# Kernel tuning notes

Measured on AMD Instinct MI355X. Metric: run time of the kernel, lower is better.

The kernel has to match this reference:

```python
import jax, jax.numpy as jnp
import numpy as np

# Dims: B=256 batch, S=512 src_len, H=512 hidden, E=256 embed, V=16000 vocab, L=1 layer
B, S, H, E, V = 256, 512, 512, 256, 16000


def setup_inputs() -> dict:
    key = jax.random.key(0)
    ks = jax.random.split(key, 12)
    inp = {
        'tgt': jax.random.randint(ks[0], (B, 1), 0, V),
        'hidden': jax.random.normal(ks[1], (1, B, H), jnp.float32),
        'cell': jax.random.normal(ks[2], (1, B, H), jnp.float32),
        'encoder_outputs': jax.random.normal(ks[3], (B, S, H), jnp.float32),
        # parameters
        'emb_table': jax.random.normal(ks[4], (V, E), jnp.float32) * 0.02,
        'attn_W': jax.random.normal(ks[5], (H, 2 * H), jnp.float32) * (1.0 / np.sqrt(2 * H)),
        'attn_b': jnp.zeros((H,), jnp.float32),
        'v': jax.random.uniform(ks[6], (H,), jnp.float32, -1.0 / np.sqrt(H), 1.0 / np.sqrt(H)),
        'W_ih': jax.random.normal(ks[7], (4 * H, E + H), jnp.float32) * (1.0 / np.sqrt(H)),
        'W_hh': jax.random.normal(ks[8], (4 * H, H), jnp.float32) * (1.0 / np.sqrt(H)),
        'b_ih': jnp.zeros((4 * H,), jnp.float32),
        'b_hh': jnp.zeros((4 * H,), jnp.float32),
        'fc_W': jax.random.normal(ks[9], (V, H), jnp.float32) * (1.0 / np.sqrt(H)),
        'fc_b': jnp.zeros((V,), jnp.float32),
    }
    return inp


def reference(tgt, hidden, cell, encoder_outputs, emb_table, attn_W, attn_b, v,
              W_ih, W_hh, b_ih, b_hh, fc_W, fc_b):
    # Embedding (dropout = identity, eval mode)  -> [B, 1, E]
    embedded = emb_table[tgt]
    h = hidden[-1]                                   # [B, H]
    c = cell[-1]                                     # [B, H]

    # Bahdanau additive attention
    Sdim = encoder_outputs.shape[1]
    h_rep = jnp.broadcast_to(h[:, None, :], (h.shape[0], Sdim, h.shape[1]))
    cat = jnp.concatenate([h_rep, encoder_outputs], axis=2)          # [B, S, 2H]
    energy = jnp.tanh(jnp.einsum('bsk,hk->bsh', cat, attn_W) + attn_b)
    scores = jnp.einsum('h,bsh->bs', v, energy)                      # [B, S]
    attn = jax.nn.softmax(scores, axis=1)                            # [B, S]

    # context = bmm(attn[:,None,:], encoder_outputs)  -> [B, H]
    context = jnp.einsum('bs,bsh->bh', attn, encoder_outputs)

    # Single-step LSTM cell (PyTorch gate order i, f, g, o)
    x = jnp.concatenate([embedded[:, 0, :], context], axis=1)        # [B, E+H]
    gates = x @ W_ih.T + b_ih + h @ W_hh.T + b_hh                    # [B, 4H]
    i, f, g, o = jnp.split(gates, 4, axis=1)
    c_new = jax.nn.sigmoid(f) * c + jax.nn.sigmoid(i) * jnp.tanh(g)
    h_new = jax.nn.sigmoid(o) * jnp.tanh(c_new)

    prediction = h_new @ fc_W.T + fc_b                               # [B, V]
    return prediction, h_new[None], c_new[None], attn[:, None, :]
```

## Files before the change

kernel.cpp:

```cpp
#include <hip/hip_runtime.h>
#include <hip/hip_bf16.h>

#define B_ 256
#define S_ 512
#define H_ 512
#define E_ 256
#define V_ 16000

typedef __attribute__((ext_vector_type(4))) float f32x4_t;
typedef __attribute__((ext_vector_type(2))) float f32x2_t;
typedef __attribute__((ext_vector_type(8))) short bf16x8_t;
typedef __attribute__((ext_vector_type(2))) unsigned u32x2_t;
typedef __attribute__((ext_vector_type(4))) unsigned u32x4_t;

#define W2_SCALE 64.0f
#define W2_INV   0.015625f

__device__ __forceinline__ bf16x8_t pack8(f32x4_t a, f32x4_t b) {
    union { unsigned u[4]; bf16x8_t v; } o;
    asm("v_cvt_pk_bf16_f32 %0, %1, %2" : "=v"(o.u[0]) : "v"(a[0]), "v"(a[1]));
    asm("v_cvt_pk_bf16_f32 %0, %1, %2" : "=v"(o.u[1]) : "v"(a[2]), "v"(a[3]));
    asm("v_cvt_pk_bf16_f32 %0, %1, %2" : "=v"(o.u[2]) : "v"(b[0]), "v"(b[1]));
    asm("v_cvt_pk_bf16_f32 %0, %1, %2" : "=v"(o.u[3]) : "v"(b[2]), "v"(b[3]));
    return o.v;
}

__device__ __forceinline__ void cvt8(short* dst, const float* src) {
    f32x4_t a = *(const f32x4_t*)src;
    f32x4_t b = *(const f32x4_t*)(src + 4);
    *(bf16x8_t*)dst = pack8(a, b);
}

__device__ __forceinline__ u32x2_t f32x8_to_fp8x8(f32x4_t a, f32x4_t b, float s) {
    unsigned d0 = 0, d1 = 0;
    d0 = __builtin_amdgcn_cvt_pk_fp8_f32(a[0] * s, a[1] * s, d0, false);
    d0 = __builtin_amdgcn_cvt_pk_fp8_f32(a[2] * s, a[3] * s, d0, true);
    d1 = __builtin_amdgcn_cvt_pk_fp8_f32(b[0] * s, b[1] * s, d1, false);
    d1 = __builtin_amdgcn_cvt_pk_fp8_f32(b[2] * s, b[3] * s, d1, true);
    u32x2_t r; r[0] = d0; r[1] = d1;
    return r;
}

__device__ __forceinline__ float tanh5(float x) {
    float e = __expf(2.f * x);
    return 1.f - 2.f * __builtin_amdgcn_rcpf(e + 1.f);
}

__device__ __forceinline__ int physc(int c, int r) {
    return ((((c & 7) << 3) | (c >> 3)) ^ (r & 7));
}

__global__ void pack_w2(const float* __restrict__ attn_W, unsigned* __restrict__ Bp)
{
    const int u    = blockIdx.x * 256 + threadIdx.x;
    const int lane = u & 63;
    const int p    = (u >> 6) & 1;
    const int wn   = (u >> 7) & 7;
    const int kk   = u >> 10;
    const int col0 = wn * 64 + (2 * p) * 16 + (lane & 15);
    const int k    = kk * 32 + (lane >> 4) * 8;
    const float* s0 = attn_W + (size_t)col0 * (2 * H_) + H_ + k;
    const float* s1 = s0 + (size_t)16 * (2 * H_);
    f32x4_t a0 = *(const f32x4_t*)s0, b0 = *(const f32x4_t*)(s0 + 4);
    f32x4_t a1 = *(const f32x4_t*)s1, b1 = *(const f32x4_t*)(s1 + 4);
    u32x2_t lo = f32x8_to_fp8x8(a0, b0, W2_SCALE);
    u32x2_t hi = f32x8_to_fp8x8(a1, b1, W2_SCALE);
    u32x4_t st; st[0] = lo[0]; st[1] = lo[1]; st[2] = hi[0]; st[3] = hi[1];
    *(u32x4_t*)(Bp + (size_t)u * 4) = st;
}

__global__ void bias1_kernel(const float* __restrict__ hidden,
                             const float* __restrict__ attn_W,
                             const float* __restrict__ attn_b,
                             float* __restrict__ bias1)
{
    const int t  = threadIdx.x;
    const int b0 = blockIdx.x * 2;
    __shared__ float h_s[2][512];
    h_s[0][t] = hidden[(size_t)b0 * H_ + t];
    h_s[1][t] = hidden[(size_t)(b0 + 1) * H_ + t];
    __syncthreads();
    const float* wrow = attn_W + (size_t)t * (2 * H_);
    float a0 = 0.f, a1 = 0.f;
#pragma unroll 4
    for (int k = 0; k < 512; k += 4) {
        f32x4_t wv = *(const f32x4_t*)(wrow + k);
        a0 = fmaf(wv[0], h_s[0][k],     a0);
        a0 = fmaf(wv[1], h_s[0][k + 1], a0);
        a0 = fmaf(wv[2], h_s[0][k + 2], a0);
        a0 = fmaf(wv[3], h_s[0][k + 3], a0);
        a1 = fmaf(wv[0], h_s[1][k],     a1);
        a1 = fmaf(wv[1], h_s[1][k + 1], a1);
        a1 = fmaf(wv[2], h_s[1][k + 2], a1);
        a1 = fmaf(wv[3], h_s[1][k + 3], a1);
    }
    const float bb = attn_b[t];
    bias1[(size_t)b0 * H_ + t]       = a0 + bb;
    bias1[(size_t)(b0 + 1) * H_ + t] = a1 + bb;
}

__global__ void fused_attn(const float* __restrict__ enc,
                           const unsigned* __restrict__ Bp,
                           const float* __restrict__ bias1,
                           const float* __restrict__ vvec,
                           float* __restrict__ e_ws,
                           float* __restrict__ lpart,
                           float* __restrict__ ctxpart)
{
    __shared__ unsigned char buf8[32 * 512];
    __shared__ float bias_s[512];
    __shared__ float v_s[512];
    __shared__ float red[32][9];
    __shared__ float e_loc[32];

    const int t    = threadIdx.x;
    const int lane = t & 63;
    const int w    = t >> 6;
    const int b    = blockIdx.x >> 4;
    const int q    = blockIdx.x & 15;

    bias_s[t] = bias1[(size_t)b * H_ + t];
    v_s[t]    = vvec[t];

    const int srow = t >> 4;
    const int sc   = t & 15;
    const float* gp = enc + ((size_t)b * S_ + q * 32 + srow) * H_ + sc * 32;
#pragma unroll
    for (int i = 0; i < 4; ++i) {
        f32x4_t a = *(const f32x4_t*)(gp + i * 8);
        f32x4_t c = *(const f32x4_t*)(gp + i * 8 + 4);
        *(u32x2_t*)&buf8[srow * 512 + physc(sc * 4 + i, srow) * 8] =
            f32x8_to_fp8x8(a, c, 1.0f);
    }
    __syncthreads();

    const int l15 = lane & 15;
    const int hi  = lane >> 4;
    const int Y   = l15 & 7;
    const unsigned char* abase = buf8 + l15 * 512 + hi * 64;
    const unsigned* bbase = Bp + (size_t)w * 512 + lane * 4;

    f32x4_t acc[2][4];
#pragma unroll
    for (int mf = 0; mf < 2; ++mf)
#pragma unroll
        for (int nf = 0; nf < 4; ++nf)
            acc[mf][nf] = (f32x4_t){0.f, 0.f, 0.f, 0.f};

#pragma unroll
    for (int kk2 = 0; kk2 < 8; ++kk2) {
        const unsigned char* ap = abase + ((kk2 ^ Y) << 3);
        const unsigned* bp = bbase + (size_t)kk2 * 8192;
#pragma unroll
        for (int par = 0; par < 2; ++par) {
            const unsigned char* app = ap + par * 256;
            const unsigned* bpp = bp + par * 4096;
            long a0 = *(const long*)(app);
            long a1 = *(const long*)(app + 8192);
            union { u32x4_t v; long l[2]; } q0, q1;
            q0.v = *(const u32x4_t*)(bpp);
            q1.v = *(const u32x4_t*)(bpp + 256);
            __builtin_amdgcn_s_setprio(1);
            acc[0][0] = __builtin_amdgcn_mfma_f32_16x16x32_fp8_fp8(a0, q0.l[0], acc[0][0], 0, 0, 0);
            acc[1][0] = __builtin_amdgcn_mfma_f32_16x16x32_fp8_fp8(a1, q0.l[0], acc[1][0], 0, 0, 0);
            acc[0][1] = __builtin_amdgcn_mfma_f32_16x16x32_fp8_fp8(a0, q0.l[1], acc[0][1], 0, 0, 0);
            acc[1][1] = __builtin_amdgcn_mfma_f32_16x16x32_fp8_fp8(a1, q0.l[1], acc[1][1], 0, 0, 0);
            acc[0][2] = __builtin_amdgcn_mfma_f32_16x16x32_fp8_fp8(a0, q1.l[0], acc[0][2], 0, 0, 0);
            acc[1][2] = __builtin_amdgcn_mfma_f32_16x16x32_fp8_fp8(a1, q1.l[0], acc[1][2], 0, 0, 0);
            acc[0][3] = __builtin_amdgcn_mfma_f32_16x16x32_fp8_fp8(a0, q1.l[1], acc[0][3], 0, 0, 0);
            acc[1][3] = __builtin_amdgcn_mfma_f32_16x16x32_fp8_fp8(a1, q1.l[1], acc[1][3], 0, 0, 0);
            __builtin_amdgcn_s_setprio(0);
        }
    }

    float part[8];
#pragma unroll
    for (int i = 0; i < 8; ++i) part[i] = 0.f;
#pragma unroll
    for (int nf = 0; nf < 4; ++nf) {
        const int col = w * 64 + nf * 16 + l15;
        const float bbv = bias_s[col];
        const float vl  = v_s[col];
#pragma unroll
        for (int mf = 0; mf < 2; ++mf)
#pragma unroll
            for (int r = 0; r < 4; ++r)
                part[mf * 4 + r] += vl * tanh5(fmaf(acc[mf][nf][r], W2_INV, bbv));
    }
#pragma unroll
    for (int i = 0; i < 8; ++i) {
        float p = part[i];
        p += __shfl_xor(p, 1);
        p += __shfl_xor(p, 2);
        p += __shfl_xor(p, 4);
        p += __shfl_xor(p, 8);
        part[i] = p;
    }
    if (l15 == 0) {
#pragma unroll
        for (int mf = 0; mf < 2; ++mf)
#pragma unroll
            for (int r = 0; r < 4; ++r)
                red[mf * 16 + (hi << 2) + r][w] = part[mf * 4 + r];
    }
    __syncthreads();

    if (t < 32) {
        float s = red[t][0] + red[t][1] + red[t][2] + red[t][3]
                + red[t][4] + red[t][5] + red[t][6] + red[t][7];
        e_loc[t] = __expf(s);
    }
    __syncthreads();

    const int cg = lane >> 3;
    const int cc = (lane & 7) * 8 + w;
    float acc8[8];
#pragma unroll
    for (int j = 0; j < 8; ++j) acc8[j] = 0.f;
#pragma unroll
    for (int i = 0; i < 4; ++i) {
        const int r   = i * 8 + cg;
        const float e = e_loc[r];
        u32x2_t ch = *(const u32x2_t*)&buf8[r * 512 + physc(cc, r) * 8];
        f32x2_t f0 = __builtin_amdgcn_cvt_pk_f32_fp8(ch[0], false);
        f32x2_t f1 = __builtin_amdgcn_cvt_pk_f32_fp8(ch[0], true);
        f32x2_t f2 = __builtin_amdgcn_cvt_pk_f32_fp8(ch[1], false);
        f32x2_t f3 = __builtin_amdgcn_cvt_pk_f32_fp8(ch[1], true);
        acc8[0] = fmaf(e, f0[0], acc8[0]);
        acc8[1] = fmaf(e, f0[1], acc8[1]);
        acc8[2] = fmaf(e, f1[0], acc8[2]);
        acc8[3] = fmaf(e, f1[1], acc8[3]);
        acc8[4] = fmaf(e, f2[0], acc8[4]);
        acc8[5] = fmaf(e, f2[1], acc8[5]);
        acc8[6] = fmaf(e, f3[0], acc8[6]);
        acc8[7] = fmaf(e, f3[1], acc8[7]);
    }
#pragma unroll
    for (int m = 8; m < 64; m <<= 1)
#pragma unroll
        for (int j = 0; j < 8; ++j)
            acc8[j] += __shfl_xor(acc8[j], m);
#pragma unroll
    for (int j = 0; j < 8; ++j)
        if (cg == j)
            ctxpart[(size_t)blockIdx.x * H_ + cc * 8 + j] = acc8[j];

    if (t < 32) {
        float sv = e_loc[t];
        sv += __shfl_xor(sv, 1);
        sv += __shfl_xor(sv, 2);
        sv += __shfl_xor(sv, 4);
        sv += __shfl_xor(sv, 8);
        sv += __shfl_xor(sv, 16);
        if (lane == 0) lpart[blockIdx.x] = sv;
        e_ws[(size_t)b * S_ + q * 32 + t] = e_loc[t];
    }
}

__global__ void combine_kernel(const float* __restrict__ e_ws,
                               const float* __restrict__ lpart,
                               const float* __restrict__ ctxpart,
                               float* __restrict__ out_attn,
                               short* __restrict__ x_cat)
{
    const int b = blockIdx.x, t = threadIdx.x;
    float l = 0.f;
#pragma unroll
    for (int j = 0; j < 16; ++j) l += lpart[16 * b + j];
    const float li = 1.f / l;
    out_attn[(size_t)b * S_ + t] = e_ws[(size_t)b * S_ + t] * li;
    float ctx = 0.f;
#pragma unroll
    for (int j = 0; j < 16; ++j)
        ctx += ctxpart[(size_t)(16 * b + j) * H_ + t];
    union { float f; unsigned u; } v; v.f = ctx * li;
    unsigned r = v.u + 0x7fffu + ((v.u >> 16) & 1u);
    x_cat[(size_t)b * 1280 + 256 + t] = (short)(r >> 16);
}

template<int KIND>
__global__ __launch_bounds__(256, 2)
void gemm_std(const short* __restrict__ Abf,
              const float* __restrict__ B0,
              const float* __restrict__ B1,
              const float* __restrict__ bias0,
              float* __restrict__ out)
{
    constexpr int K = (KIND == 0) ? 1280 : 512;
    constexpr int N = (KIND == 0) ? 2048 : 16000;
    constexpr int KITER = (KIND == 0) ? 20 : 16;

    __shared__ short As[128 * 40];
    __shared__ short Bs[128 * 40];

    const int t    = threadIdx.x;
    const int lane = t & 63;
    const int w    = t >> 6;
    const int wm   = w >> 1;
    const int wn   = w & 1;
    const int row0 = blockIdx.x * 128;
    const int col0 = blockIdx.y * 128;
    const int z    = (KIND == 0) ? blockIdx.z : 0;
    const int ks0  = z * KITER;
    float* outp    = (KIND == 0) ? out + (size_t)z * 256 * 2048 : out;

    f32x4_t acc[4][4];
#pragma unroll
    for (int i = 0; i < 4; ++i)
#pragma unroll
        for (int j = 0; j < 4; ++j)
            acc[i][j] = (f32x4_t){0.f, 0.f, 0.f, 0.f};

    const int arow = t >> 1, ah = (t & 1) * 16;
    const int bcol = t >> 1, bh = (t & 1) * 16;

    for (int ksi = 0; ksi < KITER; ++ksi) {
        const int k0 = (ks0 + ksi) * 32;
        __syncthreads();
        const short* asrc = Abf + (size_t)(row0 + arow) * K + k0 + ah;
        *(bf16x8_t*)&As[arow * 40 + ah]     = *(const bf16x8_t*)asrc;
        *(bf16x8_t*)&As[arow * 40 + ah + 8] = *(const bf16x8_t*)(asrc + 8);
        const float* bsrc;
        if constexpr (KIND == 0) {
            const int cg = col0 + bcol;
            bsrc = (k0 < 768) ? (B0 + (size_t)cg * 768 + k0 + bh)
                              : (B1 + (size_t)cg * 512 + (k0 - 768) + bh);
        } else {
            bsrc = B0 + (size_t)(col0 + bcol) * 512 + k0 + bh;
        }
        cvt8(&Bs[bcol * 40 + bh],     bsrc);
        cvt8(&Bs[bcol * 40 + bh + 8], bsrc + 8);
        __syncthreads();

        bf16x8_t af[4], bfr[4];
        const int ka = (lane >> 4) * 8;
#pragma unroll
        for (int mf = 0; mf < 4; ++mf)
            af[mf] = *(const bf16x8_t*)&As[(wm * 64 + mf * 16 + (lane & 15)) * 40 + ka];
#pragma unroll
        for (int nf = 0; nf < 4; ++nf)
            bfr[nf] = *(const bf16x8_t*)&Bs[(wn * 64 + nf * 16 + (lane & 15)) * 40 + ka];
#pragma unroll
        for (int mf = 0; mf < 4; ++mf)
#pragma unroll
            for (int nf = 0; nf < 4; ++nf)
                acc[mf][nf] = __builtin_amdgcn_mfma_f32_16x16x32_bf16(
                    af[mf], bfr[nf], acc[mf][nf], 0, 0, 0);
    }

#pragma unroll
    for (int mf = 0; mf < 4; ++mf)
#pragma unroll
        for (int nf = 0; nf < 4; ++nf) {
            const int col  = col0 + wn * 64 + nf * 16 + (lane & 15);
            const int rowb = row0 + wm * 64 + mf * 16 + ((lane >> 4) << 2);
#pragma unroll
            for (int r = 0; r < 4; ++r) {
                float v = acc[mf][nf][r];
                if constexpr (KIND == 1) v += bias0[col];
                outp[(size_t)(rowb + r) * N + col] = v;
            }
        }
}

__global__ void prep_kernel(const int* __restrict__ tgt,
                            const float* __restrict__ emb,
                            const float* __restrict__ hidden,
                            short* __restrict__ x_cat)
{
    const int b = blockIdx.x, t = threadIdx.x;
    const int tok = tgt[b];
    union { float f; unsigned u; } v0, v1, v2;
    v0.f = emb[(size_t)tok * E_ + t];
    v1.f = hidden[(size_t)b * H_ + t];
    v2.f = hidden[(size_t)b * H_ + 256 + t];
    unsigned r0 = v0.u + 0x7fffu + ((v0.u >> 16) & 1u);
    unsigned r1 = v1.u + 0x7fffu + ((v1.u >> 16) & 1u);
    unsigned r2 = v2.u + 0x7fffu + ((v2.u >> 16) & 1u);
    x_cat[(size_t)b * 1280 + t]             = (short)(r0 >> 16);
    x_cat[(size_t)b * 1280 + 768 + t]       = (short)(r1 >> 16);
    x_cat[(size_t)b * 1280 + 768 + 256 + t] = (short)(r2 >> 16);
}

__global__ void lstm_kernel(const float* __restrict__ gates0,
                            const float* __restrict__ gates1,
                            const float* __restrict__ b_ih,
                            const float* __restrict__ b_hh,
                            const float* __restrict__ cell,
                            float* __restrict__ out_h,
                            float* __restrict__ out_c,
                            short* __restrict__ h_bf)
{
    const int b = blockIdx.x, t = threadIdx.x;
    const float* g0 = gates0 + (size_t)b * 2048;
    const float* g1 = gates1 + (size_t)b * 2048;
    const float gi = g0[t]        + g1[t]        + b_ih[t]        + b_hh[t];
    const float gf = g0[512 + t]  + g1[512 + t]  + b_ih[512 + t]  + b_hh[512 + t];
    const float gg = g0[1024 + t] + g1[1024 + t] + b_ih[1024 + t] + b_hh[1024 + t];
    const float go = g0[1536 + t] + g1[1536 + t] + b_ih[1536 + t] + b_hh[1536 + t];
    const float c  = cell[(size_t)b * H_ + t];
    const float si = 1.f / (1.f + __expf(-gi));
    const float sf = 1.f / (1.f + __expf(-gf));
    const float so = 1.f / (1.f + __expf(-go));
    const float cn = sf * c + si * tanhf(gg);
    const float hn = so * tanhf(cn);
    out_h[(size_t)b * H_ + t] = hn;
    out_c[(size_t)b * H_ + t] = cn;
    union { float f; unsigned u; } v; v.f = hn;
    unsigned r = v.u + 0x7fffu + ((v.u >> 16) & 1u);
    h_bf[(size_t)b * H_ + t]  = (short)(r >> 16);
}

extern "C" void kernel_launch(void* const* d_in, const int* in_sizes, int n_in,
                              void* d_out, int out_size, void* d_ws, size_t ws_size,
                              hipStream_t stream)
{
    (void)in_sizes; (void)n_in; (void)out_size; (void)ws_size;

    const int*   tgt    = (const int*)d_in[0];
    const float* hidden = (const float*)d_in[1];
    const float* cell   = (const float*)d_in[2];
    const float* enc    = (const float*)d_in[3];
    const float* emb    = (const float*)d_in[4];
    const float* attn_W = (const float*)d_in[5];
    const float* attn_b = (const float*)d_in[6];
    const float* vv     = (const float*)d_in[7];
    const float* W_ih   = (const float*)d_in[8];
    const float* W_hh   = (const float*)d_in[9];
    const float* b_ih   = (const float*)d_in[10];
    const float* b_hh   = (const float*)d_in[11];
    const float* fc_W   = (const float*)d_in[12];
    const float* fc_b   = (const float*)d_in[13];

    float* out_pred = (float*)d_out;
    float* out_h    = out_pred + (size_t)B_ * V_;
    float* out_c    = out_h + (size_t)B_ * H_;
    float* out_attn = out_c + (size_t)B_ * H_;

    char*  ws      = (char*)d_ws;
    float* bias1   = (float*)ws;
    float* gates01 = bias1 + (size_t)B_ * H_;
    float* e_ws    = gates01 + (size_t)2 * B_ * 2048;
    float* lpart   = e_ws + (size_t)B_ * S_;
    float* ctxpart = lpart + 4096;
    short* x_cat   = (short*)(ctxpart + (size_t)4096 * H_);
    short* h_bf    = x_cat + (size_t)B_ * 1280;
    unsigned* b2p  = (unsigned*)(h_bf + (size_t)B_ * H_);

    pack_w2<<<64, 256, 0, stream>>>(attn_W, b2p);
    prep_kernel<<<B_, 256, 0, stream>>>(tgt, emb, hidden, x_cat);
    bias1_kernel<<<128, 512, 0, stream>>>(hidden, attn_W, attn_b, bias1);
    fused_attn<<<16 * B_, 512, 0, stream>>>(enc, b2p, bias1, vv, e_ws, lpart, ctxpart);
    combine_kernel<<<B_, 512, 0, stream>>>(e_ws, lpart, ctxpart, out_attn, x_cat);
    gemm_std<0><<<dim3(2, 16, 2), 256, 0, stream>>>(x_cat, W_ih, W_hh, nullptr, gates01);
    lstm_kernel<<<B_, 512, 0, stream>>>(gates01, gates01 + (size_t)B_ * 2048,
                                        b_ih, b_hh, cell, out_h, out_c, h_bf);
    gemm_std<1><<<dim3(2, 125), 256, 0, stream>>>(h_bf, fc_W, nullptr, fc_b, out_pred);
}
```

Before: 201.5 us.

## Enlarge attention tiles to 64 rows per block with 16 waves

The fused attention kernel now processes 64 source rows per block with 1024 threads instead of 32 rows with 512 threads. Each wave covers 32 hidden columns across four row fragments instead of 64 columns across two. The weight packing layout, the context reduction mapping and the combine kernel are adjusted to match. This halves the number of blocks and the per-block partial context and sum buffers, which cuts workspace traffic in the combine step and improves reuse of the weight fragments. In exchange it uses larger blocks with more LDS, which may reduce the number of blocks resident per CU.

```diff
diff --git a/kernel.cpp b/kernel.cpp
--- a/kernel.cpp
+++ b/kernel.cpp
@@ -54,10 +54,9 @@
 {
     const int u    = blockIdx.x * 256 + threadIdx.x;
     const int lane = u & 63;
-    const int p    = (u >> 6) & 1;
-    const int wn   = (u >> 7) & 7;
+    const int w    = (u >> 6) & 15;
     const int kk   = u >> 10;
-    const int col0 = wn * 64 + (2 * p) * 16 + (lane & 15);
+    const int col0 = w * 32 + (lane & 15);
     const int k    = kk * 32 + (lane >> 4) * 8;
     const float* s0 = attn_W + (size_t)col0 * (2 * H_) + H_ + k;
     const float* s1 = s0 + (size_t)16 * (2 * H_);
@@ -107,24 +106,26 @@
                            float* __restrict__ lpart,
                            float* __restrict__ ctxpart)
 {
-    __shared__ unsigned char buf8[32 * 512];
+    __shared__ unsigned char buf8[64 * 512];
     __shared__ float bias_s[512];
     __shared__ float v_s[512];
-    __shared__ float red[32][9];
-    __shared__ float e_loc[32];
+    __shared__ float red[64][17];
+    __shared__ float e_loc[64];
 
     const int t    = threadIdx.x;
     const int lane = t & 63;
     const int w    = t >> 6;
-    const int b    = blockIdx.x >> 4;
-    const int q    = blockIdx.x & 15;
-
-    bias_s[t] = bias1[(size_t)b * H_ + t];
-    v_s[t]    = vvec[t];
+    const int b    = blockIdx.x >> 3;
+    const int q    = blockIdx.x & 7;
+
+    if (t < 512) {
+        bias_s[t] = bias1[(size_t)b * H_ + t];
+        v_s[t]    = vvec[t];
+    }
 
     const int srow = t >> 4;
     const int sc   = t & 15;
-    const float* gp = enc + ((size_t)b * S_ + q * 32 + srow) * H_ + sc * 32;
+    const float* gp = enc + ((size_t)b * S_ + q * 64 + srow) * H_ + sc * 32;
 #pragma unroll
     for (int i = 0; i < 4; ++i) {
         f32x4_t a = *(const f32x4_t*)(gp + i * 8);
@@ -138,14 +139,14 @@
     const int hi  = lane >> 4;
     const int Y   = l15 & 7;
     const unsigned char* abase = buf8 + l15 * 512 + hi * 64;
-    const unsigned* bbase = Bp + (size_t)w * 512 + lane * 4;
-
-    f32x4_t acc[2][4];
-#pragma unroll
-    for (int mf = 0; mf < 2; ++mf)
-#pragma unroll
-        for (int nf = 0; nf < 4; ++nf)
-            acc[mf][nf] = (f32x4_t){0.f, 0.f, 0.f, 0.f};
+    const unsigned* bbase = Bp + (size_t)w * 256 + lane * 4;
+
+    f32x4_t acc[4][2];
+#pragma unroll
+    for (int mf = 0; mf < 4; ++mf) {
+        acc[mf][0] = (f32x4_t){0.f, 0.f, 0.f, 0.f};
+        acc[mf][1] = (f32x4_t){0.f, 0.f, 0.f, 0.f};
+    }
 
 #pragma unroll
     for (int kk2 = 0; kk2 < 8; ++kk2) {
@@ -154,41 +155,41 @@
 #pragma unroll
         for (int par = 0; par < 2; ++par) {
             const unsigned char* app = ap + par * 256;
-            const unsigned* bpp = bp + par * 4096;
+            union { u32x4_t v; long l[2]; } q0;
+            q0.v = *(const u32x4_t*)(bp + par * 4096);
             long a0 = *(const long*)(app);
             long a1 = *(const long*)(app + 8192);
-            union { u32x4_t v; long l[2]; } q0, q1;
-            q0.v = *(const u32x4_t*)(bpp);
-            q1.v = *(const u32x4_t*)(bpp + 256);
+            long a2 = *(const long*)(app + 16384);
+            long a3 = *(const long*)(app + 24576);
             __builtin_amdgcn_s_setprio(1);
             acc[0][0] = __builtin_amdgcn_mfma_f32_16x16x32_fp8_fp8(a0, q0.l[0], acc[0][0], 0, 0, 0);
             acc[1][0] = __builtin_amdgcn_mfma_f32_16x16x32_fp8_fp8(a1, q0.l[0], acc[1][0], 0, 0, 0);
+            acc[2][0] = __builtin_amdgcn_mfma_f32_16x16x32_fp8_fp8(a2, q0.l[0], acc[2][0], 0, 0, 0);
+            acc[3][0] = __builtin_amdgcn_mfma_f32_16x16x32_fp8_fp8(a3, q0.l[0], acc[3][0], 0, 0, 0);
             acc[0][1] = __builtin_amdgcn_mfma_f32_16x16x32_fp8_fp8(a0, q0.l[1], acc[0][1], 0, 0, 0);
             acc[1][1] = __builtin_amdgcn_mfma_f32_16x16x32_fp8_fp8(a1, q0.l[1], acc[1][1], 0, 0, 0);
-            acc[0][2] = __builtin_amdgcn_mfma_f32_16x16x32_fp8_fp8(a0, q1.l[0], acc[0][2], 0, 0, 0);
-            acc[1][2] = __builtin_amdgcn_mfma_f32_16x16x32_fp8_fp8(a1, q1.l[0], acc[1][2], 0, 0, 0);
-            acc[0][3] = __builtin_amdgcn_mfma_f32_16x16x32_fp8_fp8(a0, q1.l[1], acc[0][3], 0, 0, 0);
-            acc[1][3] = __builtin_amdgcn_mfma_f32_16x16x32_fp8_fp8(a1, q1.l[1], acc[1][3], 0, 0, 0);
+            acc[2][1] = __builtin_amdgcn_mfma_f32_16x16x32_fp8_fp8(a2, q0.l[1], acc[2][1], 0, 0, 0);
+            acc[3][1] = __builtin_amdgcn_mfma_f32_16x16x32_fp8_fp8(a3, q0.l[1], acc[3][1], 0, 0, 0);
             __builtin_amdgcn_s_setprio(0);
         }
     }
 
-    float part[8];
-#pragma unroll
-    for (int i = 0; i < 8; ++i) part[i] = 0.f;
-#pragma unroll
-    for (int nf = 0; nf < 4; ++nf) {
-        const int col = w * 64 + nf * 16 + l15;
+    float part[16];
+#pragma unroll
+    for (int i = 0; i < 16; ++i) part[i] = 0.f;
+#pragma unroll
+    for (int nf = 0; nf < 2; ++nf) {
+        const int col = w * 32 + nf * 16 + l15;
         const float bbv = bias_s[col];
         const float vl  = v_s[col];
 #pragma unroll
-        for (int mf = 0; mf < 2; ++mf)
+        for (int mf = 0; mf < 4; ++mf)
 #pragma unroll
             for (int r = 0; r < 4; ++r)
                 part[mf * 4 + r] += vl * tanh5(fmaf(acc[mf][nf][r], W2_INV, bbv));
     }
 #pragma unroll
-    for (int i = 0; i < 8; ++i) {
+    for (int i = 0; i < 16; ++i) {
         float p = part[i];
         p += __shfl_xor(p, 1);
         p += __shfl_xor(p, 2);
@@ -198,28 +199,29 @@
     }
     if (l15 == 0) {
 #pragma unroll
-        for (int mf = 0; mf < 2; ++mf)
+        for (int mf = 0; mf < 4; ++mf)
 #pragma unroll
             for (int r = 0; r < 4; ++r)
                 red[mf * 16 + (hi << 2) + r][w] = part[mf * 4 + r];
     }
     __syncthreads();
 
-    if (t < 32) {
-        float s = red[t][0] + red[t][1] + red[t][2] + red[t][3]
-                + red[t][4] + red[t][5] + red[t][6] + red[t][7];
+    if (t < 64) {
+        float s = 0.f;
+#pragma unroll
+        for (int g = 0; g < 16; ++g) s += red[t][g];
         e_loc[t] = __expf(s);
     }
     __syncthreads();
 
-    const int cg = lane >> 3;
-    const int cc = (lane & 7) * 8 + w;
+    const int cc = t >> 4;
+    const int rg = t & 15;
     float acc8[8];
 #pragma unroll
     for (int j = 0; j < 8; ++j) acc8[j] = 0.f;
 #pragma unroll
     for (int i = 0; i < 4; ++i) {
-        const int r   = i * 8 + cg;
+        const int r   = i * 16 + rg;
         const float e = e_loc[r];
         u32x2_t ch = *(const u32x2_t*)&buf8[r * 512 + physc(cc, r) * 8];
         f32x2_t f0 = __builtin_amdgcn_cvt_pk_f32_fp8(ch[0], false);
@@ -236,24 +238,25 @@
         acc8[7] = fmaf(e, f3[1], acc8[7]);
     }
 #pragma unroll
-    for (int m = 8; m < 64; m <<= 1)
+    for (int m = 1; m < 16; m <<= 1)
 #pragma unroll
         for (int j = 0; j < 8; ++j)
             acc8[j] += __shfl_xor(acc8[j], m);
 #pragma unroll
     for (int j = 0; j < 8; ++j)
-        if (cg == j)
+        if (rg == j)
             ctxpart[(size_t)blockIdx.x * H_ + cc * 8 + j] = acc8[j];
 
-    if (t < 32) {
+    if (t < 64) {
         float sv = e_loc[t];
         sv += __shfl_xor(sv, 1);
         sv += __shfl_xor(sv, 2);
         sv += __shfl_xor(sv, 4);
         sv += __shfl_xor(sv, 8);
         sv += __shfl_xor(sv, 16);
+        sv += __shfl_xor(sv, 32);
         if (lane == 0) lpart[blockIdx.x] = sv;
-        e_ws[(size_t)b * S_ + q * 32 + t] = e_loc[t];
+        e_ws[(size_t)b * S_ + q * 64 + t] = e_loc[t];
     }
 }
 
@@ -266,13 +269,13 @@
     const int b = blockIdx.x, t = threadIdx.x;
     float l = 0.f;
 #pragma unroll
-    for (int j = 0; j < 16; ++j) l += lpart[16 * b + j];
+    for (int j = 0; j < 8; ++j) l += lpart[8 * b + j];
     const float li = 1.f / l;
     out_attn[(size_t)b * S_ + t] = e_ws[(size_t)b * S_ + t] * li;
     float ctx = 0.f;
 #pragma unroll
-    for (int j = 0; j < 16; ++j)
-        ctx += ctxpart[(size_t)(16 * b + j) * H_ + t];
+    for (int j = 0; j < 8; ++j)
+        ctx += ctxpart[(size_t)(8 * b + j) * H_ + t];
     union { float f; unsigned u; } v; v.f = ctx * li;
     unsigned r = v.u + 0x7fffu + ((v.u >> 16) & 1u);
     x_cat[(size_t)b * 1280 + 256 + t] = (short)(r >> 16);
@@ -442,15 +445,15 @@
     float* gates01 = bias1 + (size_t)B_ * H_;
     float* e_ws    = gates01 + (size_t)2 * B_ * 2048;
     float* lpart   = e_ws + (size_t)B_ * S_;
-    float* ctxpart = lpart + 4096;
-    short* x_cat   = (short*)(ctxpart + (size_t)4096 * H_);
+    float* ctxpart = lpart + 2048;
+    short* x_cat   = (short*)(ctxpart + (size_t)2048 * H_);
     short* h_bf    = x_cat + (size_t)B_ * 1280;
     unsigned* b2p  = (unsigned*)(h_bf + (size_t)B_ * H_);
 
     pack_w2<<<64, 256, 0, stream>>>(attn_W, b2p);
     prep_kernel<<<B_, 256, 0, stream>>>(tgt, emb, hidden, x_cat);
     bias1_kernel<<<128, 512, 0, stream>>>(hidden, attn_W, attn_b, bias1);
-    fused_attn<<<16 * B_, 512, 0, stream>>>(enc, b2p, bias1, vv, e_ws, lpart, ctxpart);
+    fused_attn<<<8 * B_, 1024, 0, stream>>>(enc, b2p, bias1, vv, e_ws, lpart, ctxpart);
     combine_kernel<<<B_, 512, 0, stream>>>(e_ws, lpart, ctxpart, out_attn, x_cat);
     gemm_std<0><<<dim3(2, 16, 2), 256, 0, stream>>>(x_cat, W_ih, W_hh, nullptr, gates01);
     lstm_kernel<<<B_, 512, 0, stream>>>(gates01, gates01 + (size_t)B_ * 2048,
```

Result: slower. 234.0 us (+16.2%).
